# Performance work log

Hardware: AMD Instinct MI355X
Metric: run time of the kernel (lower is better)

The kernel has to match this reference:

```python
import jax, jax.numpy as jnp
import numpy as np

B, LQ, LV = 32, 64, 128
QS, FS, BN = 512, 1024, 512

def setup_inputs() -> dict:
    key = jax.random.key(0)
    k1, k2, k3, k4, k5 = jax.random.split(key, 5)
    s = lambda n: 1.0 / np.sqrt(n)
    return {
        "phr_feats": jax.random.normal(k1, (B, LQ, QS), dtype=jnp.float32),
        "vis_feats": jax.random.normal(k2, (B, LV, FS), dtype=jnp.float32),
        "W": jax.random.uniform(k3, (BN, QS), jnp.float32, -s(QS), s(QS)),
        "U": jax.random.uniform(k4, (BN, FS), jnp.float32, -s(FS), s(FS)),
        "b": jnp.ones((BN,), dtype=jnp.float32),
        "w": jax.random.uniform(k5, (1, BN), jnp.float32, -s(BN), s(BN)),
    }

def reference(phr_feats, vis_feats, W, U, b, w):
    # Wh: [B,Lq,BN], Uv: [B,Lv,BN]
    Wh = jnp.einsum('bqd,nd->bqn', phr_feats, W)
    Uv = jnp.einsum('bvf,nf->bvn', vis_feats, U)
    # broadcast add + tanh: [B,Lq,Lv,BN]
    t = jnp.tanh(Wh[:, :, None, :] + Uv[:, None, :, :] + b)
    energies = jnp.einsum('bqvn,n->bqv', t, w[0])  # squeeze(-1)
    weights = jax.nn.softmax(energies, axis=2)
    aligned = jnp.einsum('bqv,bvf->bqf', weights, vis_feats)
    semantic_group_feats = jnp.concatenate([phr_feats, aligned], axis=2)
    return (semantic_group_feats, weights, energies)
```

## Files before the change

### kernel.cpp

```cpp
#include <hip/hip_runtime.h>

#define NB  32
#define NLQ 64
#define NLV 128
#define NQS 512
#define NFS 1024
#define NBN 512
#define CC  2.8853900817779268f

typedef float  floatx4 __attribute__((ext_vector_type(4)));
typedef __bf16 bf16x8  __attribute__((ext_vector_type(8)));
typedef unsigned short us;
typedef __attribute__((address_space(1))) const unsigned int gu32;
typedef __attribute__((address_space(3))) unsigned int lu32;

__device__ __forceinline__ us f2bf(float f) {
    unsigned int u = __float_as_uint(f);
    u += 0x7fffu + ((u >> 16) & 1u);
    return (us)(u >> 16);
}
__device__ __forceinline__ unsigned int pktrunc(float lo, float hi) {
    return __builtin_amdgcn_perm(__float_as_uint(hi), __float_as_uint(lo), 0x07060302u);
}
__device__ __forceinline__ float blo(unsigned int u) {
    return __uint_as_float(u << 16);
}
__device__ __forceinline__ float bhi(unsigned int u) {
    return __uint_as_float(u & 0xffff0000u);
}

#define PHR4 262144
#define VIS4 1048576
#define WW4  65536
#define UU4  131072
#define TOT4 (PHR4 + VIS4 + WW4 + UU4)

__global__ __launch_bounds__(256) void convert_bf16(
    const float* __restrict__ phr, const float* __restrict__ vis,
    const float* __restrict__ W,   const float* __restrict__ U,
    us* __restrict__ phr_b, us* __restrict__ vis_b,
    us* __restrict__ W_b,   us* __restrict__ U_b,
    float* __restrict__ out_sgf)
{
    int i = blockIdx.x * 256 + threadIdx.x;
    if (i >= TOT4) return;
    const float* src; us* dst; int o;
    if (i < PHR4)              { src = phr; dst = phr_b; o = i; }
    else if (i < PHR4 + VIS4)  { src = vis; dst = vis_b; o = i - PHR4; }
    else if (i < PHR4 + VIS4 + WW4) { src = W; dst = W_b; o = i - PHR4 - VIS4; }
    else                       { src = U; dst = U_b; o = i - PHR4 - VIS4 - WW4; }
    float4 v = ((const float4*)src)[o];
    uint2 r = { pktrunc(v.x, v.y), pktrunc(v.z, v.w) };
    *(uint2*)(dst + (size_t)o * 4) = r;
    if (i < PHR4) {
        int row = o >> 7, c4 = o & 127;
        ((float4*)out_sgf)[(size_t)row * 384 + c4] = v;
    }
}

__device__ __forceinline__ void gemm64(
    us* smem,
    const us* __restrict__ A, const us* __restrict__ Bt,
    const float* __restrict__ bias,
    float* __restrict__ whYp, us* __restrict__ uvYTp,
    int K, int bx, int by)
{
    us* As = smem;
    us* Bs = smem + 2048;
    const int tid  = threadIdx.x;
    const int m0   = bx * 64;
    const int n0   = by * 64;
    const int wave = tid >> 6;
    const int lane = tid & 63;
    const int wm   = (wave >> 1) * 32;
    const int wn   = (wave & 1) * 32;
    const int fm   = lane & 15;
    const int c16  = lane >> 4;

    const int srow   = tid >> 2;
    const int scol16 = ((tid & 3) - srow - (srow >> 2)) & 3;
    const us* ga = A  + (size_t)(m0 + srow) * K + scol16 * 8;
    const us* gb = Bt + (size_t)(n0 + srow) * K + scol16 * 8;

    floatx4 acc[2][2] = {};
    for (int k0 = 0; k0 < K; k0 += 32) {
        __syncthreads();
        __builtin_amdgcn_global_load_lds((gu32*)(ga + k0),
                                         (lu32*)(As + wave * 512), 16, 0, 0);
        __builtin_amdgcn_global_load_lds((gu32*)(gb + k0),
                                         (lu32*)(Bs + wave * 512), 16, 0, 0);
        __syncthreads();
        bf16x8 am[2], bn[2];
        #pragma unroll
        for (int i = 0; i < 2; ++i) {
            int r  = wm + 16 * i + fm;
            int sl = (c16 + r + (r >> 2)) & 3;
            am[i] = *(const bf16x8*)(As + r * 32 + sl * 8);
        }
        #pragma unroll
        for (int j = 0; j < 2; ++j) {
            int r  = wn + 16 * j + fm;
            int sl = (c16 + r + (r >> 2)) & 3;
            bn[j] = *(const bf16x8*)(Bs + r * 32 + sl * 8);
        }
        #pragma unroll
        for (int i = 0; i < 2; ++i)
            #pragma unroll
            for (int j = 0; j < 2; ++j)
                acc[i][j] = __builtin_amdgcn_mfma_f32_16x16x32_bf16(am[i], bn[j], acc[i][j], 0, 0, 0);
    }

    const int cr = (lane >> 4) * 4;
    const int cc = lane & 15;
    if (whYp) {
        #pragma unroll
        for (int j = 0; j < 2; ++j) {
            int gn = n0 + wn + 16 * j + cc;
            float bj = bias[gn];
            #pragma unroll
            for (int i = 0; i < 2; ++i)
                #pragma unroll
                for (int r = 0; r < 4; ++r) {
                    int gm = m0 + wm + 16 * i + cr + r;
                    whYp[(size_t)gm * NBN + gn] =
                        __builtin_amdgcn_exp2f(CC * (acc[i][j][r] + bj));
                }
        }
    } else {
        us* Cs = smem;
        __syncthreads();
        #pragma unroll
        for (int i = 0; i < 2; ++i)
            #pragma unroll
            for (int j = 0; j < 2; ++j) {
                int nl = wn + 16 * j + cc;
                int vl = wm + 16 * i + cr;
                #pragma unroll
                for (int r = 0; r < 4; ++r)
                    Cs[nl * 72 + vl + r] =
                        f2bf(__builtin_amdgcn_exp2f(CC * acc[i][j][r]));
            }
        __syncthreads();
        const int bb    = m0 >> 7;
        const int vbase = m0 & 127;
        const int nl    = tid >> 2;
        const int vc    = (tid & 3) * 16;
        uint4 t0 = *(const uint4*)(Cs + nl * 72 + vc);
        uint4 t1 = *(const uint4*)(Cs + nl * 72 + vc + 8);
        us* dst = uvYTp + ((size_t)bb * NBN + n0 + nl) * NLV + vbase + vc;
        *(uint4*)dst       = t0;
        *(uint4*)(dst + 8) = t1;
    }
}

__global__ __launch_bounds__(256) void gemm_both(
    const us* __restrict__ phr_b, const us* __restrict__ W_b,
    const float* __restrict__ bias,
    const us* __restrict__ vis_b, const us* __restrict__ U_b,
    float* __restrict__ whY, us* __restrict__ uvYT)
{
    __shared__ __align__(16) us smem[4608];
    int blk = blockIdx.x;
    if (blk < 256) {
        int bx = blk % 32, by = blk / 32;
        gemm64(smem, phr_b, W_b, bias, whY, nullptr, NQS, bx, by);
    } else {
        blk -= 256;
        int bx = blk % 64, by = blk / 64;
        gemm64(smem, vis_b, U_b, bias, nullptr, uvYT, NFS, bx, by);
    }
}

__global__ __launch_bounds__(512) void energize(
    const float* __restrict__ whY,
    const us* __restrict__ uvYT,
    const float* __restrict__ wvec,
    float* __restrict__ out_w, float* __restrict__ out_e,
    us* __restrict__ p_bf, us* __restrict__ p_lo)
{
    const float LOG2E = 1.4426950408889634f;
    int blk = blockIdx.x;
    blk = (blk & 7) * 64 + (blk >> 3);
    const int b    = blk >> 4;
    const int qq4  = blk & 15;
    const int tid  = threadIdx.x;
    const int wave = __builtin_amdgcn_readfirstlane(tid >> 6);
    const int lane = tid & 63;
    const int q0   = qq4 * 4;

    __shared__ float part[4][8][NLV];

    float4 sw0 = *(const float4*)(wvec + lane * 8);
    float4 sw1 = *(const float4*)(wvec + lane * 8 + 4);
    float sumw = sw0.x + sw0.y + sw0.z + sw0.w + sw1.x + sw1.y + sw1.z + sw1.w;
    #pragma unroll
    for (int off = 32; off; off >>= 1) sumw += __shfl_xor(sumw, off);

    const float* yqp = whY + (size_t)(b * NLQ + q0) * NBN + wave * 64;
    const float* wp  = wvec + wave * 64;
    const us*    uvp = uvYT + ((size_t)b * NBN + wave * 64) * NLV + 2 * lane;

    float acc[4][2] = {};
    #pragma unroll 2
    for (int nc = 0; nc < 64; nc += 8) {
        unsigned int yv[8];
        #pragma unroll
        for (int k = 0; k < 8; ++k)
            yv[k] = *(const unsigned int*)(uvp + (size_t)(nc + k) * NLV);
        #pragma unroll
        for (int kk = 0; kk < 4; ++kk) {
            const int k0 = nc + 2 * kk, k1 = k0 + 1;
            float x0a = blo(yv[2 * kk]),     x0b = bhi(yv[2 * kk]);
            float x1a = blo(yv[2 * kk + 1]), x1b = bhi(yv[2 * kk + 1]);
            float w0 = wp[k0], w1 = wp[k1];
            #pragma unroll
            for (int q = 0; q < 4; ++q) {
                float y0 = yqp[q * NBN + k0];
                float y1 = yqp[q * NBN + k1];
                float d0a = fmaf(x0a, y0, 1.f), d1a = fmaf(x1a, y1, 1.f);
                float d0b = fmaf(x0b, y0, 1.f), d1b = fmaf(x1b, y1, 1.f);
                float numa = fmaf(w0, d1a, w1 * d0a);
                float numb = fmaf(w0, d1b, w1 * d0b);
                acc[q][0] = fmaf(numa, __builtin_amdgcn_rcpf(d0a * d1a), acc[q][0]);
                acc[q][1] = fmaf(numb, __builtin_amdgcn_rcpf(d0b * d1b), acc[q][1]);
            }
        }
    }
    #pragma unroll
    for (int q = 0; q < 4; ++q) {
        float2 t = { acc[q][0], acc[q][1] };
        *(float2*)&part[q][wave][2 * lane] = t;
    }
    __syncthreads();

    if (wave < 4) {
        const int q = wave;
        float s0 = 0.f, s1 = 0.f;
        #pragma unroll
        for (int nq = 0; nq < 8; ++nq) {
            s0 += part[q][nq][2 * lane];
            s1 += part[q][nq][2 * lane + 1];
        }
        float e0 = sumw - 2.f * s0;
        float e1 = sumw - 2.f * s1;
        float m = fmaxf(e0, e1);
        #pragma unroll
        for (int off = 32; off; off >>= 1) m = fmaxf(m, __shfl_xor(m, off));
        float x0 = __builtin_amdgcn_exp2f((e0 - m) * LOG2E);
        float x1 = __builtin_amdgcn_exp2f((e1 - m) * LOG2E);
        float ss = x0 + x1;
        #pragma unroll
        for (int off = 32; off; off >>= 1) ss += __shfl_xor(ss, off);
        float inv = __builtin_amdgcn_rcpf(ss);
        float p0 = x0 * inv, p1 = x1 * inv;

        const size_t row = (size_t)(b * NLQ + q0 + q);
        float2 ep = { e0, e1 };
        float2 pp = { p0, p1 };
        *(float2*)(out_e + row * NLV + 2 * lane) = ep;
        *(float2*)(out_w + row * NLV + 2 * lane) = pp;
        unsigned int pb0 = f2bf(p0), pb1 = f2bf(p1);
        float lo0 = p0 - __uint_as_float(pb0 << 16);
        float lo1 = p1 - __uint_as_float(pb1 << 16);
        unsigned int lb0 = f2bf(lo0), lb1 = f2bf(lo1);
        *(unsigned int*)(p_bf + row * NLV + 2 * lane) = pb0 | (pb1 << 16);
        *(unsigned int*)(p_lo + row * NLV + 2 * lane) = lb0 | (lb1 << 16);
    }
}

__global__ __launch_bounds__(256) void aligned_mfma(
    const us* __restrict__ p_bf, const us* __restrict__ p_lo,
    const us* __restrict__ vis_b,
    float* __restrict__ out_sgf)
{
    int blk = blockIdx.x;
    blk = (blk & 7) * 64 + (blk >> 3);
    const int b    = blk >> 4;
    const int ft   = blk & 15;
    const int tid  = threadIdx.x;
    const int wave = tid >> 6;
    const int lane = tid & 63;
    const int wm   = (wave >> 1) * 32;
    const int wf   = (wave & 1) * 32;
    const int fm   = lane & 15;
    const int fko  = (lane >> 4) * 8;

    __shared__ us Vs[64][136];

    {
        const int v  = tid >> 1;
        const int fh = (tid & 1) * 32;
        const us* vp = vis_b + ((size_t)b * NLV + v) * NFS + ft * 64 + fh;
        #pragma unroll
        for (int r = 0; r < 8; ++r) {
            uint2 u = *(const uint2*)(vp + 4 * r);
            Vs[fh + 4 * r + 0][v] = (us)(u.x & 0xffffu);
            Vs[fh + 4 * r + 1][v] = (us)(u.x >> 16);
            Vs[fh + 4 * r + 2][v] = (us)(u.y & 0xffffu);
            Vs[fh + 4 * r + 3][v] = (us)(u.y >> 16);
        }
    }
    __syncthreads();

    floatx4 acc[2][2] = {};
    const us* pA  = p_bf + ((size_t)b * NLQ + wm + fm) * NLV + fko;
    const us* pAl = p_lo + ((size_t)b * NLQ + wm + fm) * NLV + fko;

    #pragma unroll
    for (int ks = 0; ks < 4; ++ks) {
        bf16x8 a[2], al[2], bb2[2];
        #pragma unroll
        for (int i = 0; i < 2; ++i) {
            a[i]  = *(const bf16x8*)(pA  + (size_t)i * 16 * NLV + ks * 32);
            al[i] = *(const bf16x8*)(pAl + (size_t)i * 16 * NLV + ks * 32);
        }
        #pragma unroll
        for (int j = 0; j < 2; ++j)
            bb2[j] = *(const bf16x8*)&Vs[wf + 16 * j + fm][ks * 32 + fko];
        #pragma unroll
        for (int i = 0; i < 2; ++i)
            #pragma unroll
            for (int j = 0; j < 2; ++j) {
                acc[i][j] = __builtin_amdgcn_mfma_f32_16x16x32_bf16(a[i],  bb2[j], acc[i][j], 0, 0, 0);
                acc[i][j] = __builtin_amdgcn_mfma_f32_16x16x32_bf16(al[i], bb2[j], acc[i][j], 0, 0, 0);
            }
    }

    const int cr = (lane >> 4) * 4;
    const int cc = lane & 15;
    #pragma unroll
    for (int i = 0; i < 2; ++i)
        #pragma unroll
        for (int j = 0; j < 2; ++j)
            #pragma unroll
            for (int r = 0; r < 4; ++r) {
                int q = wm + 16 * i + cr + r;
                int f = ft * 64 + wf + 16 * j + cc;
                size_t row = (size_t)b * NLQ + q;
                out_sgf[row * (NQS + NFS) + NQS + f] = acc[i][j][r];
            }
}

extern "C" void kernel_launch(void* const* d_in, const int* in_sizes, int n_in,
                              void* d_out, int out_size, void* d_ws, size_t ws_size,
                              hipStream_t stream) {
    const float* phr  = (const float*)d_in[0];
    const float* vis  = (const float*)d_in[1];
    const float* W    = (const float*)d_in[2];
    const float* U    = (const float*)d_in[3];
    const float* bias = (const float*)d_in[4];
    const float* wvec = (const float*)d_in[5];

    char* ws = (char*)d_ws;
    us* phr_b   = (us*)ws;
    us* vis_b   = (us*)(ws + (2u << 20));
    us* W_b     = (us*)(ws + (10u << 20));
    us* U_b     = (us*)(ws + (10u << 20) + (512u << 10));
    float* whY  = (float*)(ws + (12u << 20));
    us* uvYT    = (us*)(ws + (16u << 20));
    us* p_bf    = (us*)(ws + (20u << 20));
    us* p_lo    = (us*)(ws + (20u << 20) + (512u << 10));

    float* out     = (float*)d_out;
    float* out_sgf = out;
    float* out_w   = out_sgf + (size_t)NB * NLQ * (NQS + NFS);
    float* out_e   = out_w   + (size_t)NB * NLQ * NLV;

    convert_bf16<<<TOT4 / 256, 256, 0, stream>>>(
        phr, vis, W, U, phr_b, vis_b, W_b, U_b, out_sgf);
    gemm_both<<<768, 256, 0, stream>>>(phr_b, W_b, bias, vis_b, U_b, whY, uvYT);
    energize<<<512, 512, 0, stream>>>(whY, uvYT, wvec, out_w, out_e, p_bf, p_lo);
    aligned_mfma<<<512, 256, 0, stream>>>(p_bf, p_lo, vis_b, out_sgf);
}
```

Measured before the change: 125.4 us.

## Double-buffer GEMM LDS tiles with K=64 steps and XOR swizzle

Turns the projection GEMM main loop into a double-buffered pipeline. The next K tile's global-to-LDS loads are issued before the MFMAs on the current tile, and the K step grows from 32 to 64 with an XOR-based bank swizzle. This removes one barrier per iteration and hides global load latency behind compute. In exchange, LDS per block grows to 32KB, which may lower occupancy, and the pre-epilogue barrier is removed on the assumption that the loop's trailing sync covers it.

```diff
diff --git a/kernel.cpp b/kernel.cpp
--- a/kernel.cpp
+++ b/kernel.cpp
@@ -65,8 +65,6 @@
     float* __restrict__ whYp, us* __restrict__ uvYTp,
     int K, int bx, int by)
 {
-    us* As = smem;
-    us* Bs = smem + 2048;
     const int tid  = threadIdx.x;
     const int m0   = bx * 64;
     const int n0   = by * 64;
@@ -77,38 +75,58 @@
     const int fm   = lane & 15;
     const int c16  = lane >> 4;
 
-    const int srow   = tid >> 2;
-    const int scol16 = ((tid & 3) - srow - (srow >> 2)) & 3;
-    const us* ga = A  + (size_t)(m0 + srow) * K + scol16 * 8;
-    const us* gb = Bt + (size_t)(n0 + srow) * K + scol16 * 8;
+    const int r0 = tid >> 3;
+    const int lc = (tid & 7) ^ (r0 & 7);
+    const us* ga0 = A  + (size_t)(m0 + r0)      * K + lc * 8;
+    const us* ga1 = A  + (size_t)(m0 + r0 + 32) * K + lc * 8;
+    const us* gb0 = Bt + (size_t)(n0 + r0)      * K + lc * 8;
+    const us* gb1 = Bt + (size_t)(n0 + r0 + 32) * K + lc * 8;
+    const int dst0 = wave * 512;
+    const int dst1 = 2048 + wave * 512;
 
     floatx4 acc[2][2] = {};
-    for (int k0 = 0; k0 < K; k0 += 32) {
+    const int nt = K >> 6;
+    int cur = 0;
+
+#define STAGE(bufbase, k0) do {                                                \
+    us* as_ = (bufbase);  us* bs_ = (bufbase) + 4096;                          \
+    __builtin_amdgcn_global_load_lds((gu32*)(ga0 + (k0)), (lu32*)(as_ + dst0), 16, 0, 0); \
+    __builtin_amdgcn_global_load_lds((gu32*)(ga1 + (k0)), (lu32*)(as_ + dst1), 16, 0, 0); \
+    __builtin_amdgcn_global_load_lds((gu32*)(gb0 + (k0)), (lu32*)(bs_ + dst0), 16, 0, 0); \
+    __builtin_amdgcn_global_load_lds((gu32*)(gb1 + (k0)), (lu32*)(bs_ + dst1), 16, 0, 0); \
+} while (0)
+
+    STAGE(smem, 0);
+    __syncthreads();
+    for (int t = 0; t < nt; ++t) {
+        us* As = smem + cur * 8192;
+        us* Bs = As + 4096;
+        if (t + 1 < nt) STAGE(smem + (cur ^ 1) * 8192, (t + 1) * 64);
+        #pragma unroll
+        for (int ks = 0; ks < 2; ++ks) {
+            bf16x8 am[2], bn[2];
+            #pragma unroll
+            for (int i = 0; i < 2; ++i) {
+                int r  = wm + 16 * i + fm;
+                int pc = (ks * 4 + c16) ^ (r & 7);
+                am[i] = *(const bf16x8*)(As + r * 64 + pc * 8);
+            }
+            #pragma unroll
+            for (int j = 0; j < 2; ++j) {
+                int r  = wn + 16 * j + fm;
+                int pc = (ks * 4 + c16) ^ (r & 7);
+                bn[j] = *(const bf16x8*)(Bs + r * 64 + pc * 8);
+            }
+            #pragma unroll
+            for (int i = 0; i < 2; ++i)
+                #pragma unroll
+                for (int j = 0; j < 2; ++j)
+                    acc[i][j] = __builtin_amdgcn_mfma_f32_16x16x32_bf16(am[i], bn[j], acc[i][j], 0, 0, 0);
+        }
         __syncthreads();
-        __builtin_amdgcn_global_load_lds((gu32*)(ga + k0),
-                                         (lu32*)(As + wave * 512), 16, 0, 0);
-        __builtin_amdgcn_global_load_lds((gu32*)(gb + k0),
-                                         (lu32*)(Bs + wave * 512), 16, 0, 0);
-        __syncthreads();
-        bf16x8 am[2], bn[2];
-        #pragma unroll
-        for (int i = 0; i < 2; ++i) {
-            int r  = wm + 16 * i + fm;
-            int sl = (c16 + r + (r >> 2)) & 3;
-            am[i] = *(const bf16x8*)(As + r * 32 + sl * 8);
-        }
-        #pragma unroll
-        for (int j = 0; j < 2; ++j) {
-            int r  = wn + 16 * j + fm;
-            int sl = (c16 + r + (r >> 2)) & 3;
-            bn[j] = *(const bf16x8*)(Bs + r * 32 + sl * 8);
-        }
-        #pragma unroll
-        for (int i = 0; i < 2; ++i)
-            #pragma unroll
-            for (int j = 0; j < 2; ++j)
-                acc[i][j] = __builtin_amdgcn_mfma_f32_16x16x32_bf16(am[i], bn[j], acc[i][j], 0, 0, 0);
-    }
+        cur ^= 1;
+    }
+#undef STAGE
 
     const int cr = (lane >> 4) * 4;
     const int cc = lane & 15;
@@ -128,7 +146,6 @@
         }
     } else {
         us* Cs = smem;
-        __syncthreads();
         #pragma unroll
         for (int i = 0; i < 2; ++i)
             #pragma unroll
@@ -159,7 +176,7 @@
     const us* __restrict__ vis_b, const us* __restrict__ U_b,
     float* __restrict__ whY, us* __restrict__ uvYT)
 {
-    __shared__ __align__(16) us smem[4608];
+    __shared__ __align__(16) us smem[16384];
     int blk = blockIdx.x;
     if (blk < 256) {
         int bx = blk % 32, by = blk / 32;
```

New measurement: 118.9 us. -5.2%, faster.
